# Kernel tuning notes

Measured on AMD Instinct MI355X. Metric: run time of the kernel, lower is better.

Reference implementation:

```python
import jax, jax.numpy as jnp
import numpy as np

E, L, R, H, V = 8, 8, 4, 4096, 32000
B, S = 2, 1024


def setup_inputs() -> dict:
    key = jax.random.key(0)
    ks = jax.random.split(key, 8)
    scale = 0.02
    return {
        "hidden_state": jax.random.normal(ks[0], (B, S, H), jnp.float32),
        "router_w": jax.random.normal(ks[1], (E, H), jnp.float32) * scale,
        "router_b": jnp.zeros((E,), jnp.float32),
        "expert_B": jax.random.normal(ks[2], (E, L, R, H), jnp.float32) * scale,
        "expert_A": jax.random.normal(ks[3], (E, L, H, R), jnp.float32) * scale,
        "deep_B": jax.random.normal(ks[4], (L, R, H), jnp.float32) * scale,
        "deep_A": jax.random.normal(ks[5], (L, H, R), jnp.float32) * scale,
        "lm_head_w": jax.random.normal(ks[6], (V, H), jnp.float32) * scale,
    }


def reference(hidden_state, router_w, router_b, expert_B, expert_A,
              deep_B, deep_A, lm_head_w):
    h = hidden_state  # [B,S,H]
    # Router applies softmax internally; forward softmaxes AGAIN (faithful to source).
    router_logits = jax.nn.softmax(
        jnp.einsum('bsh,eh->bse', h, router_w) + router_b, axis=-1)
    router_probs = jax.nn.softmax(router_logits, axis=-1)  # [B,S,E]
    psum = jnp.sum(router_probs, axis=-1, keepdims=True)   # [B,S,1] (== 1)

    n_layers = deep_B.shape[0]
    for i in range(n_layers):
        # All experts' LoRA low-rank projections in one batched contraction.
        z = jnp.einsum('bsh,erh->bser', h, expert_B[:, i])  # [B,S,E,r]
        # combined = sum_e p_e * (h + z_e @ A_e^T) = h * sum_e p_e + weighted delta
        zw = z * router_probs[..., None]                    # [B,S,E,r]
        delta = jnp.einsum('bser,ehr->bsh', zw, expert_A[:, i])
        combined = h * psum + delta                         # [B,S,H]
        # Residual deep LoRA merge: x + (x @ B^T) @ A^T
        low = jnp.einsum('bsh,rh->bsr', combined, deep_B[i])
        h = combined + jnp.einsum('bsr,hr->bsh', low, deep_A[i])

    lm_logits = jnp.einsum('bsh,vh->bsv', h, lm_head_w)  # [B,S,V]
    return (lm_logits, router_logits)
```

## Files before the change

kernel.cpp:

```cpp
#include <hip/hip_runtime.h>
#include <cstdint>
#include <cstddef>

#define HD 4096
#define EE 8
#define LL 8
#define RR 4
#define VV 32000
#define NTOK 2048
#define NKT (HD / 64)

typedef __attribute__((ext_vector_type(8))) short bf16x8;
typedef __attribute__((ext_vector_type(4))) float f32x4;

static __device__ __forceinline__ unsigned short f2bf(float f) {
    unsigned int u = __builtin_bit_cast(unsigned int, f);
    unsigned int r = (u + 0x7FFFu + ((u >> 16) & 1u)) >> 16;
    return (unsigned short)r;
}

__global__ __launch_bounds__(256) void fused_layers(
    const float* __restrict__ h_in,
    const float* __restrict__ router_w,
    const float* __restrict__ router_b,
    const float* __restrict__ expert_B,
    const float* __restrict__ expert_A,
    const float* __restrict__ deep_B,
    const float* __restrict__ deep_A,
    float* __restrict__ router_logits,
    unsigned short* __restrict__ h_out)
{
    __shared__ float h_lds[4][HD];
    __shared__ float zw_lds[4][32];
    __shared__ float probs_lds[4][EE];
    __shared__ float psum_lds[4];
    __shared__ float red[4][4][4];
    __shared__ float low_lds[4][4];

    const int tid  = threadIdx.x;
    const int lane = tid & 63;
    const int wv   = tid >> 6;
    const int t0   = blockIdx.x * 4;

    for (int t = 0; t < 4; ++t) {
        const float4* src = (const float4*)(h_in + (size_t)(t0 + t) * HD);
        float4* dst = (float4*)h_lds[t];
        #pragma unroll
        for (int q = 0; q < 4; ++q) dst[tid + q * 256] = src[tid + q * 256];
    }
    __syncthreads();

    {
        float racc[EE];
        #pragma unroll
        for (int e = 0; e < EE; ++e) racc[e] = 0.f;
        for (int k = 0; k < HD / 64; ++k) {
            int pos = lane + k * 64;
            float hv = h_lds[wv][pos];
            #pragma unroll
            for (int e = 0; e < EE; ++e) racc[e] += hv * router_w[e * HD + pos];
        }
        #pragma unroll
        for (int e = 0; e < EE; ++e)
            for (int m = 1; m < 64; m <<= 1) racc[e] += __shfl_xor(racc[e], m);
        if (lane == 0) {
            float lg[EE], mx = -1e30f;
            #pragma unroll
            for (int e = 0; e < EE; ++e) { lg[e] = racc[e] + router_b[e]; mx = fmaxf(mx, lg[e]); }
            float s = 0.f;
            #pragma unroll
            for (int e = 0; e < EE; ++e) { lg[e] = expf(lg[e] - mx); s += lg[e]; }
            float inv = 1.f / s;
            float p1[EE], mx2 = -1e30f;
            #pragma unroll
            for (int e = 0; e < EE; ++e) { p1[e] = lg[e] * inv; mx2 = fmaxf(mx2, p1[e]); }
            float s2 = 0.f, q2[EE];
            #pragma unroll
            for (int e = 0; e < EE; ++e) { q2[e] = expf(p1[e] - mx2); s2 += q2[e]; }
            float inv2 = 1.f / s2, ps = 0.f;
            #pragma unroll
            for (int e = 0; e < EE; ++e) {
                float p2 = q2[e] * inv2;
                probs_lds[wv][e] = p2;
                ps += p2;
                router_logits[(size_t)(t0 + wv) * EE + e] = p1[e];
            }
            psum_lds[wv] = ps;
        }
    }
    __syncthreads();

    for (int li = 0; li < LL; ++li) {
        {
            float zacc[8][4] = {};
            const float* bp[8];
            #pragma unroll
            for (int j = 0; j < 8; ++j) {
                int er = wv * 8 + j;
                int e = er >> 2, r = er & 3;
                bp[j] = expert_B + (size_t)(e * LL + li) * (RR * HD) + (size_t)r * HD;
            }
            for (int k = 0; k < 64; ++k) {
                int pos = lane + k * 64;
                float hv0 = h_lds[0][pos], hv1 = h_lds[1][pos];
                float hv2 = h_lds[2][pos], hv3 = h_lds[3][pos];
                #pragma unroll
                for (int j = 0; j < 8; ++j) {
                    float wt = bp[j][pos];
                    zacc[j][0] += wt * hv0; zacc[j][1] += wt * hv1;
                    zacc[j][2] += wt * hv2; zacc[j][3] += wt * hv3;
                }
            }
            #pragma unroll
            for (int j = 0; j < 8; ++j)
                #pragma unroll
                for (int t = 0; t < 4; ++t) {
                    float v = zacc[j][t];
                    for (int m = 1; m < 64; m <<= 1) v += __shfl_xor(v, m);
                    zacc[j][t] = v;
                }
            if (lane == 0) {
                #pragma unroll
                for (int j = 0; j < 8; ++j) {
                    int er = wv * 8 + j;
                    #pragma unroll
                    for (int t = 0; t < 4; ++t)
                        zw_lds[t][er] = zacc[j][t] * probs_lds[t][er >> 2];
                }
            }
        }
        __syncthreads();

        float dacc[4][16] = {};
        const int pbase = wv * 1024 + lane;
        for (int e = 0; e < EE; ++e) {
            float zwt[4][4];
            #pragma unroll
            for (int t = 0; t < 4; ++t)
                #pragma unroll
                for (int r = 0; r < RR; ++r) zwt[t][r] = zw_lds[t][e * 4 + r];
            const float4* ap = (const float4*)expert_A + (size_t)(e * LL + li) * HD;
            #pragma unroll
            for (int it = 0; it < 16; ++it) {
                float4 a4 = ap[pbase + it * 64];
                #pragma unroll
                for (int t = 0; t < 4; ++t)
                    dacc[t][it] += zwt[t][0] * a4.x + zwt[t][1] * a4.y +
                                   zwt[t][2] * a4.z + zwt[t][3] * a4.w;
            }
        }

        float lowacc[4][4] = {};
        float psv[4];
        #pragma unroll
        for (int t = 0; t < 4; ++t) psv[t] = psum_lds[t];
        const float* dbp = deep_B + (size_t)li * (RR * HD);
        #pragma unroll
        for (int it = 0; it < 16; ++it) {
            int pos = pbase + it * 64;
            float db0 = dbp[pos], db1 = dbp[HD + pos], db2 = dbp[2 * HD + pos], db3 = dbp[3 * HD + pos];
            #pragma unroll
            for (int t = 0; t < 4; ++t) {
                float c = h_lds[t][pos] * psv[t] + dacc[t][it];
                h_lds[t][pos] = c;
                lowacc[t][0] += c * db0; lowacc[t][1] += c * db1;
                lowacc[t][2] += c * db2; lowacc[t][3] += c * db3;
            }
        }
        #pragma unroll
        for (int t = 0; t < 4; ++t)
            #pragma unroll
            for (int r = 0; r < RR; ++r) {
                float v = lowacc[t][r];
                for (int m = 1; m < 64; m <<= 1) v += __shfl_xor(v, m);
                lowacc[t][r] = v;
            }
        if (lane == 0) {
            #pragma unroll
            for (int t = 0; t < 4; ++t)
                #pragma unroll
                for (int r = 0; r < RR; ++r) red[wv][t][r] = lowacc[t][r];
        }
        __syncthreads();
        if (tid < 16) {
            int t = tid >> 2, r = tid & 3;
            low_lds[t][r] = red[0][t][r] + red[1][t][r] + red[2][t][r] + red[3][t][r];
        }
        __syncthreads();

        {
            float lw[4][4];
            #pragma unroll
            for (int t = 0; t < 4; ++t)
                #pragma unroll
                for (int r = 0; r < RR; ++r) lw[t][r] = low_lds[t][r];
            const float4* dap = (const float4*)deep_A + (size_t)li * HD;
            #pragma unroll
            for (int it = 0; it < 16; ++it) {
                int pos = pbase + it * 64;
                float4 a4 = dap[pos];
                #pragma unroll
                for (int t = 0; t < 4; ++t)
                    h_lds[t][pos] += lw[t][0] * a4.x + lw[t][1] * a4.y +
                                     lw[t][2] * a4.z + lw[t][3] * a4.w;
            }
        }
        __syncthreads();
    }

    for (int t = 0; t < 4; ++t) {
        ushort4* dst = (ushort4*)(h_out + (size_t)(t0 + t) * HD);
        const float4* src = (const float4*)h_lds[t];
        #pragma unroll
        for (int q = 0; q < 4; ++q) {
            int c = tid + q * 256;
            float4 v = src[c];
            ushort4 o;
            o.x = f2bf(v.x); o.y = f2bf(v.y); o.z = f2bf(v.z); o.w = f2bf(v.w);
            dst[c] = o;
        }
    }
}

__global__ __launch_bounds__(256) void cvt_kernel(const float4* __restrict__ in,
                                                  ushort4* __restrict__ out, int n4)
{
    int i = blockIdx.x * 256 + threadIdx.x;
    int stride = gridDim.x * 256;
    for (; i < n4; i += stride) {
        float4 v = in[i];
        ushort4 o;
        o.x = f2bf(v.x); o.y = f2bf(v.y); o.z = f2bf(v.z); o.w = f2bf(v.w);
        out[i] = o;
    }
}

#define GLD(src, dst) __builtin_amdgcn_global_load_lds( \
    (const __attribute__((address_space(1))) unsigned int*)(src), \
    (__attribute__((address_space(3))) unsigned int*)(dst), 16, 0, 0)

#define STAGE(pp, matoff, bufv, hh, ktv) do { \
    char* db_ = smem + (bufv) * 65536 + (matoff) + (hh) * 16384 + wv * 1024; \
    GLD(pp[0] + (size_t)(hh) * (128ull * HD * 2) + (size_t)(ktv) * 128, db_); \
    GLD(pp[1] + (size_t)(hh) * (128ull * HD * 2) + (size_t)(ktv) * 128, db_ + 8192); \
} while (0)

#define LDSREAD(off) (*(const bf16x8*)(smem + (off)))

__global__ __launch_bounds__(512, 2) void lm_gemm256(
    const unsigned short* __restrict__ A,
    const unsigned short* __restrict__ Bw,
    float* __restrict__ C)
{
    __shared__ __attribute__((aligned(128))) char smem[131072];

    const int bid = blockIdx.x;
    const int swz = (bid & 7) * 125 + (bid >> 3);
    const int bm = swz & 7;
    const int bn = swz >> 3;

    const int tid  = threadIdx.x;
    const int lane = tid & 63;
    const int wv   = tid >> 6;
    const int wr   = wv >> 2;
    const int wc   = wv & 3;

    const char* pA[2];
    const char* pB[2];
    #pragma unroll
    for (int q = 0; q < 2; ++q) {
        int off = (q * 512 + tid) * 16;
        int p = off ^ (((off >> 9) & 1) << 5);
        int st = p >> 10;
        int r  = (st >> 1) * 16 + ((p >> 6) & 15);
        int cb = (st & 1) * 64 + (p & 63);
        pA[q] = (const char*)(A  + (size_t)(bm * 256 + r) * HD) + cb;
        pB[q] = (const char*)(Bw + (size_t)(bn * 256 + r) * HD) + cb;
    }

    const int xlane = ((lane >> 3) & 1) << 5;
    const int abase = ((wr * 8) << 11) + ((lane & 15) << 6) + ((lane >> 4) << 4);
    const int bbase = 32768 + ((wc * 4) << 11) + ((lane & 15) << 6) + ((lane >> 4) << 4);

    f32x4 acc[8][4] = {};
    bf16x8 aF[4][2], bF0[2][2], bF1[2][2];

    STAGE(pB, 32768, 0, 0, 0);
    STAGE(pB, 32768, 0, 1, 0);
    STAGE(pA, 0,     0, 0, 0);
    STAGE(pA, 0,     0, 1, 0);
    STAGE(pB, 32768, 1, 0, 1);
    STAGE(pB, 32768, 1, 1, 1);
    asm volatile("s_waitcnt vmcnt(4)" ::: "memory");
    __builtin_amdgcn_s_barrier();
    __builtin_amdgcn_sched_barrier(0);

    #pragma unroll 2
    for (int kt = 0; kt < NKT; ++kt) {
        const int cur = kt & 1;
        const int oth = cur ^ 1;
        const int cb0 = cur << 16;

        #pragma unroll
        for (int i = 0; i < 4; ++i)
            #pragma unroll
            for (int ks = 0; ks < 2; ++ks)
                aF[i][ks] = LDSREAD(cb0 + ((abase + (i << 11) + (ks << 10)) ^ xlane));
        #pragma unroll
        for (int n = 0; n < 2; ++n)
            #pragma unroll
            for (int ks = 0; ks < 2; ++ks)
                bF0[n][ks] = LDSREAD(cb0 + ((bbase + (n << 11) + (ks << 10)) ^ xlane));
        if (kt + 1 < NKT) STAGE(pA, 0, oth, 0, kt + 1);
        __builtin_amdgcn_s_barrier();
        __builtin_amdgcn_sched_barrier(0);
        __builtin_amdgcn_s_setprio(1);
        #pragma unroll
        for (int ks = 0; ks < 2; ++ks)
            #pragma unroll
            for (int i = 0; i < 4; ++i)
                #pragma unroll
                for (int n = 0; n < 2; ++n)
                    acc[i][n] = __builtin_amdgcn_mfma_f32_16x16x32_bf16(
                        aF[i][ks], bF0[n][ks], acc[i][n], 0, 0, 0);
        __builtin_amdgcn_s_setprio(0);
        __builtin_amdgcn_s_barrier();
        __builtin_amdgcn_sched_barrier(0);

        #pragma unroll
        for (int n = 0; n < 2; ++n)
            #pragma unroll
            for (int ks = 0; ks < 2; ++ks)
                bF1[n][ks] = LDSREAD(cb0 + ((bbase + ((n + 2) << 11) + (ks << 10)) ^ xlane));
        if (kt + 1 < NKT) STAGE(pA, 0, oth, 1, kt + 1);
        __builtin_amdgcn_s_barrier();
        __builtin_amdgcn_sched_barrier(0);
        __builtin_amdgcn_s_setprio(1);
        #pragma unroll
        for (int ks = 0; ks < 2; ++ks)
            #pragma unroll
            for (int i = 0; i < 4; ++i)
                #pragma unroll
                for (int n = 0; n < 2; ++n)
                    acc[i][n + 2] = __builtin_amdgcn_mfma_f32_16x16x32_bf16(
                        aF[i][ks], bF1[n][ks], acc[i][n + 2], 0, 0, 0);
        __builtin_amdgcn_s_setprio(0);
        __builtin_amdgcn_s_barrier();
        __builtin_amdgcn_sched_barrier(0);

        #pragma unroll
        for (int i = 0; i < 4; ++i)
            #pragma unroll
            for (int ks = 0; ks < 2; ++ks)
                aF[i][ks] = LDSREAD(cb0 + ((abase + ((i + 4) << 11) + (ks << 10)) ^ xlane));
        if (kt + 2 < NKT) STAGE(pB, 32768, cur, 0, kt + 2);
        __builtin_amdgcn_s_barrier();
        __builtin_amdgcn_sched_barrier(0);
        __builtin_amdgcn_s_setprio(1);
        #pragma unroll
        for (int ks = 0; ks < 2; ++ks)
            #pragma unroll
            for (int i = 0; i < 4; ++i)
                #pragma unroll
                for (int n = 0; n < 2; ++n)
                    acc[i + 4][n + 2] = __builtin_amdgcn_mfma_f32_16x16x32_bf16(
                        aF[i][ks], bF1[n][ks], acc[i + 4][n + 2], 0, 0, 0);
        __builtin_amdgcn_s_setprio(0);
        __builtin_amdgcn_s_barrier();
        __builtin_amdgcn_sched_barrier(0);

        if (kt + 2 < NKT) {
            STAGE(pB, 32768, cur, 1, kt + 2);
            asm volatile("s_waitcnt vmcnt(4)" ::: "memory");
        } else {
            asm volatile("s_waitcnt vmcnt(0)" ::: "memory");
        }
        __builtin_amdgcn_s_barrier();
        __builtin_amdgcn_sched_barrier(0);
        __builtin_amdgcn_s_setprio(1);
        #pragma unroll
        for (int ks = 0; ks < 2; ++ks)
            #pragma unroll
            for (int i = 0; i < 4; ++i)
                #pragma unroll
                for (int n = 0; n < 2; ++n)
                    acc[i + 4][n] = __builtin_amdgcn_mfma_f32_16x16x32_bf16(
                        aF[i][ks], bF0[n][ks], acc[i + 4][n], 0, 0, 0);
        __builtin_amdgcn_s_setprio(0);
        __builtin_amdgcn_s_barrier();
        __builtin_amdgcn_sched_barrier(0);
    }

    const int crow0 = bm * 256 + wr * 128 + ((lane >> 4) << 2);
    const int ccol0 = bn * 256 + wc * 64 + (lane & 15);
    #pragma unroll
    for (int fm = 0; fm < 8; ++fm)
        #pragma unroll
        for (int fn = 0; fn < 4; ++fn) {
            int row = crow0 + fm * 16;
            int col = ccol0 + fn * 16;
            #pragma unroll
            for (int j = 0; j < 4; ++j)
                C[(size_t)(row + j) * VV + col] = acc[fm][fn][j];
        }
}

extern "C" void kernel_launch(void* const* d_in, const int* in_sizes, int n_in,
                              void* d_out, int out_size, void* d_ws, size_t ws_size,
                              hipStream_t stream) {
    const float* h_in      = (const float*)d_in[0];
    const float* router_w  = (const float*)d_in[1];
    const float* router_b  = (const float*)d_in[2];
    const float* expert_B  = (const float*)d_in[3];
    const float* expert_A  = (const float*)d_in[4];
    const float* deep_B    = (const float*)d_in[5];
    const float* deep_A    = (const float*)d_in[6];
    const float* lm_head_w = (const float*)d_in[7];

    float* out = (float*)d_out;
    float* router_logits_out = out + (size_t)NTOK * VV;

    unsigned short* h_bf = (unsigned short*)d_ws;
    unsigned short* w_bf = (unsigned short*)((char*)d_ws + (size_t)NTOK * HD * 2);

    fused_layers<<<dim3(NTOK / 4), dim3(256), 0, stream>>>(
        h_in, router_w, router_b, expert_B, expert_A, deep_B, deep_A,
        router_logits_out, h_bf);

    cvt_kernel<<<dim3(4096), dim3(256), 0, stream>>>(
        (const float4*)lm_head_w, (ushort4*)w_bf, VV * HD / 4);

    lm_gemm256<<<dim3((NTOK / 256) * (VV / 256)), dim3(512), 0, stream>>>(
        h_bf, w_bf, out);
}
```

Before: 1.068 ms.

## Fuse weight conversion into layer kernel and prefetch B fragments in GEMM

Merges the lm_head fp32-to-bf16 conversion kernel into the per-token layer kernel, with blocks split by index between conversion and layer work, so both run concurrently and one launch is dropped. The layer kernel moves to 512 threads with float4 vectorised loads for the router and expert_B projections, halving per-wave work. Separately, the GEMM double-buffers the bF0 fragments and loads the next tile's B fragments early to hide LDS latency. The risks are higher register pressure in the GEMM and load imbalance between conversion and layer blocks.

```diff
diff --git a/kernel.cpp b/kernel.cpp
--- a/kernel.cpp
+++ b/kernel.cpp
@@ -9,6 +9,7 @@
 #define VV 32000
 #define NTOK 2048
 #define NKT (HD / 64)
+#define CVTB 2048
 
 typedef __attribute__((ext_vector_type(8))) short bf16x8;
 typedef __attribute__((ext_vector_type(4))) float f32x4;
@@ -19,7 +20,7 @@
     return (unsigned short)r;
 }
 
-__global__ __launch_bounds__(256) void fused_layers(
+__global__ __launch_bounds__(512, 4) void fused_all(
     const float* __restrict__ h_in,
     const float* __restrict__ router_w,
     const float* __restrict__ router_b,
@@ -28,37 +29,58 @@
     const float* __restrict__ deep_B,
     const float* __restrict__ deep_A,
     float* __restrict__ router_logits,
-    unsigned short* __restrict__ h_out)
+    unsigned short* __restrict__ h_out,
+    const float4* __restrict__ lm_w,
+    ushort4* __restrict__ w_bf)
 {
     __shared__ float h_lds[4][HD];
     __shared__ float zw_lds[4][32];
     __shared__ float probs_lds[4][EE];
     __shared__ float psum_lds[4];
-    __shared__ float red[4][4][4];
+    __shared__ float red[8][4][4];
     __shared__ float low_lds[4][4];
 
-    const int tid  = threadIdx.x;
+    const int bid = blockIdx.x;
+    const int tid = threadIdx.x;
+
+    if (!((bid < 1024) && ((bid & 1) == 0))) {
+        const int ci = (bid < 1024) ? (bid >> 1) : (512 + (bid - 1024));
+        const int n4 = VV * HD / 4;
+        const int stride = CVTB * 512;
+        for (int i = ci * 512 + tid; i < n4; i += stride) {
+            float4 v = lm_w[i];
+            ushort4 o;
+            o.x = f2bf(v.x); o.y = f2bf(v.y); o.z = f2bf(v.z); o.w = f2bf(v.w);
+            w_bf[i] = o;
+        }
+        return;
+    }
+
     const int lane = tid & 63;
     const int wv   = tid >> 6;
-    const int t0   = blockIdx.x * 4;
+    const int t0   = (bid >> 1) * 4;
 
     for (int t = 0; t < 4; ++t) {
         const float4* src = (const float4*)(h_in + (size_t)(t0 + t) * HD);
         float4* dst = (float4*)h_lds[t];
         #pragma unroll
-        for (int q = 0; q < 4; ++q) dst[tid + q * 256] = src[tid + q * 256];
+        for (int q = 0; q < 2; ++q) dst[tid + q * 512] = src[tid + q * 512];
     }
     __syncthreads();
 
-    {
+    if (wv < 4) {
         float racc[EE];
         #pragma unroll
         for (int e = 0; e < EE; ++e) racc[e] = 0.f;
-        for (int k = 0; k < HD / 64; ++k) {
-            int pos = lane + k * 64;
-            float hv = h_lds[wv][pos];
-            #pragma unroll
-            for (int e = 0; e < EE; ++e) racc[e] += hv * router_w[e * HD + pos];
+        const float4* h4 = (const float4*)h_lds[wv];
+        for (int k4 = 0; k4 < HD / 256; ++k4) {
+            int idx = lane + k4 * 64;
+            float4 hv = h4[idx];
+            #pragma unroll
+            for (int e = 0; e < EE; ++e) {
+                float4 w4 = ((const float4*)(router_w + e * HD))[idx];
+                racc[e] += w4.x * hv.x + w4.y * hv.y + w4.z * hv.z + w4.w * hv.w;
+            }
         }
         #pragma unroll
         for (int e = 0; e < EE; ++e)
@@ -92,27 +114,32 @@
 
     for (int li = 0; li < LL; ++li) {
         {
-            float zacc[8][4] = {};
-            const float* bp[8];
-            #pragma unroll
-            for (int j = 0; j < 8; ++j) {
-                int er = wv * 8 + j;
+            float zacc[4][4] = {};
+            const float4* bp4[4];
+            #pragma unroll
+            for (int j = 0; j < 4; ++j) {
+                int er = wv * 4 + j;
                 int e = er >> 2, r = er & 3;
-                bp[j] = expert_B + (size_t)(e * LL + li) * (RR * HD) + (size_t)r * HD;
-            }
-            for (int k = 0; k < 64; ++k) {
-                int pos = lane + k * 64;
-                float hv0 = h_lds[0][pos], hv1 = h_lds[1][pos];
-                float hv2 = h_lds[2][pos], hv3 = h_lds[3][pos];
-                #pragma unroll
-                for (int j = 0; j < 8; ++j) {
-                    float wt = bp[j][pos];
-                    zacc[j][0] += wt * hv0; zacc[j][1] += wt * hv1;
-                    zacc[j][2] += wt * hv2; zacc[j][3] += wt * hv3;
+                bp4[j] = (const float4*)(expert_B + (size_t)((e * LL + li) * RR + r) * HD);
+            }
+            const float4* h40 = (const float4*)h_lds[0];
+            const float4* h41 = (const float4*)h_lds[1];
+            const float4* h42 = (const float4*)h_lds[2];
+            const float4* h43 = (const float4*)h_lds[3];
+            for (int k4 = 0; k4 < HD / 256; ++k4) {
+                int idx = lane + k4 * 64;
+                float4 hv0 = h40[idx], hv1 = h41[idx], hv2 = h42[idx], hv3 = h43[idx];
+                #pragma unroll
+                for (int j = 0; j < 4; ++j) {
+                    float4 w4 = bp4[j][idx];
+                    zacc[j][0] += w4.x * hv0.x + w4.y * hv0.y + w4.z * hv0.z + w4.w * hv0.w;
+                    zacc[j][1] += w4.x * hv1.x + w4.y * hv1.y + w4.z * hv1.z + w4.w * hv1.w;
+                    zacc[j][2] += w4.x * hv2.x + w4.y * hv2.y + w4.z * hv2.z + w4.w * hv2.w;
+                    zacc[j][3] += w4.x * hv3.x + w4.y * hv3.y + w4.z * hv3.z + w4.w * hv3.w;
                 }
             }
             #pragma unroll
-            for (int j = 0; j < 8; ++j)
+            for (int j = 0; j < 4; ++j)
                 #pragma unroll
                 for (int t = 0; t < 4; ++t) {
                     float v = zacc[j][t];
@@ -121,8 +148,8 @@
                 }
             if (lane == 0) {
                 #pragma unroll
-                for (int j = 0; j < 8; ++j) {
-                    int er = wv * 8 + j;
+                for (int j = 0; j < 4; ++j) {
+                    int er = wv * 4 + j;
                     #pragma unroll
                     for (int t = 0; t < 4; ++t)
                         zw_lds[t][er] = zacc[j][t] * probs_lds[t][er >> 2];
@@ -131,8 +158,8 @@
         }
         __syncthreads();
 
-        float dacc[4][16] = {};
-        const int pbase = wv * 1024 + lane;
+        float dacc[4][8] = {};
+        const int pbase = wv * 512 + lane;
         for (int e = 0; e < EE; ++e) {
             float zwt[4][4];
             #pragma unroll
@@ -141,7 +168,7 @@
                 for (int r = 0; r < RR; ++r) zwt[t][r] = zw_lds[t][e * 4 + r];
             const float4* ap = (const float4*)expert_A + (size_t)(e * LL + li) * HD;
             #pragma unroll
-            for (int it = 0; it < 16; ++it) {
+            for (int it = 0; it < 8; ++it) {
                 float4 a4 = ap[pbase + it * 64];
                 #pragma unroll
                 for (int t = 0; t < 4; ++t)
@@ -156,7 +183,7 @@
         for (int t = 0; t < 4; ++t) psv[t] = psum_lds[t];
         const float* dbp = deep_B + (size_t)li * (RR * HD);
         #pragma unroll
-        for (int it = 0; it < 16; ++it) {
+        for (int it = 0; it < 8; ++it) {
             int pos = pbase + it * 64;
             float db0 = dbp[pos], db1 = dbp[HD + pos], db2 = dbp[2 * HD + pos], db3 = dbp[3 * HD + pos];
             #pragma unroll
@@ -184,7 +211,10 @@
         __syncthreads();
         if (tid < 16) {
             int t = tid >> 2, r = tid & 3;
-            low_lds[t][r] = red[0][t][r] + red[1][t][r] + red[2][t][r] + red[3][t][r];
+            float s = 0.f;
+            #pragma unroll
+            for (int w = 0; w < 8; ++w) s += red[w][t][r];
+            low_lds[t][r] = s;
         }
         __syncthreads();
 
@@ -196,7 +226,7 @@
                 for (int r = 0; r < RR; ++r) lw[t][r] = low_lds[t][r];
             const float4* dap = (const float4*)deep_A + (size_t)li * HD;
             #pragma unroll
-            for (int it = 0; it < 16; ++it) {
+            for (int it = 0; it < 8; ++it) {
                 int pos = pbase + it * 64;
                 float4 a4 = dap[pos];
                 #pragma unroll
@@ -212,26 +242,13 @@
         ushort4* dst = (ushort4*)(h_out + (size_t)(t0 + t) * HD);
         const float4* src = (const float4*)h_lds[t];
         #pragma unroll
-        for (int q = 0; q < 4; ++q) {
-            int c = tid + q * 256;
+        for (int q = 0; q < 2; ++q) {
+            int c = tid + q * 512;
             float4 v = src[c];
             ushort4 o;
             o.x = f2bf(v.x); o.y = f2bf(v.y); o.z = f2bf(v.z); o.w = f2bf(v.w);
             dst[c] = o;
         }
-    }
-}
-
-__global__ __launch_bounds__(256) void cvt_kernel(const float4* __restrict__ in,
-                                                  ushort4* __restrict__ out, int n4)
-{
-    int i = blockIdx.x * 256 + threadIdx.x;
-    int stride = gridDim.x * 256;
-    for (; i < n4; i += stride) {
-        float4 v = in[i];
-        ushort4 o;
-        o.x = f2bf(v.x); o.y = f2bf(v.y); o.z = f2bf(v.z); o.w = f2bf(v.w);
-        out[i] = o;
     }
 }
 
@@ -283,7 +300,7 @@
     const int bbase = 32768 + ((wc * 4) << 11) + ((lane & 15) << 6) + ((lane >> 4) << 4);
 
     f32x4 acc[8][4] = {};
-    bf16x8 aF[4][2], bF0[2][2], bF1[2][2];
+    bf16x8 aF[4][2], bF0[2][2][2], bF1[2][2];
 
     STAGE(pB, 32768, 0, 0, 0);
     STAGE(pB, 32768, 0, 1, 0);
@@ -294,6 +311,11 @@
     asm volatile("s_waitcnt vmcnt(4)" ::: "memory");
     __builtin_amdgcn_s_barrier();
     __builtin_amdgcn_sched_barrier(0);
+    #pragma unroll
+    for (int n = 0; n < 2; ++n)
+        #pragma unroll
+        for (int ks = 0; ks < 2; ++ks)
+            bF0[0][n][ks] = LDSREAD(((bbase + (n << 11) + (ks << 10)) ^ xlane));
 
     #pragma unroll 2
     for (int kt = 0; kt < NKT; ++kt) {
@@ -306,11 +328,6 @@
             #pragma unroll
             for (int ks = 0; ks < 2; ++ks)
                 aF[i][ks] = LDSREAD(cb0 + ((abase + (i << 11) + (ks << 10)) ^ xlane));
-        #pragma unroll
-        for (int n = 0; n < 2; ++n)
-            #pragma unroll
-            for (int ks = 0; ks < 2; ++ks)
-                bF0[n][ks] = LDSREAD(cb0 + ((bbase + (n << 11) + (ks << 10)) ^ xlane));
         if (kt + 1 < NKT) STAGE(pA, 0, oth, 0, kt + 1);
         __builtin_amdgcn_s_barrier();
         __builtin_amdgcn_sched_barrier(0);
@@ -322,7 +339,7 @@
                 #pragma unroll
                 for (int n = 0; n < 2; ++n)
                     acc[i][n] = __builtin_amdgcn_mfma_f32_16x16x32_bf16(
-                        aF[i][ks], bF0[n][ks], acc[i][n], 0, 0, 0);
+                        aF[i][ks], bF0[cur][n][ks], acc[i][n], 0, 0, 0);
         __builtin_amdgcn_s_setprio(0);
         __builtin_amdgcn_s_barrier();
         __builtin_amdgcn_sched_barrier(0);
@@ -377,6 +394,14 @@
         }
         __builtin_amdgcn_s_barrier();
         __builtin_amdgcn_sched_barrier(0);
+        if (kt + 1 < NKT) {
+            const int nb0 = oth << 16;
+            #pragma unroll
+            for (int n = 0; n < 2; ++n)
+                #pragma unroll
+                for (int ks = 0; ks < 2; ++ks)
+                    bF0[oth][n][ks] = LDSREAD(nb0 + ((bbase + (n << 11) + (ks << 10)) ^ xlane));
+        }
         __builtin_amdgcn_s_setprio(1);
         #pragma unroll
         for (int ks = 0; ks < 2; ++ks)
@@ -385,7 +410,7 @@
                 #pragma unroll
                 for (int n = 0; n < 2; ++n)
                     acc[i + 4][n] = __builtin_amdgcn_mfma_f32_16x16x32_bf16(
-                        aF[i][ks], bF0[n][ks], acc[i + 4][n], 0, 0, 0);
+                        aF[i][ks], bF0[cur][n][ks], acc[i + 4][n], 0, 0, 0);
         __builtin_amdgcn_s_setprio(0);
         __builtin_amdgcn_s_barrier();
         __builtin_amdgcn_sched_barrier(0);
@@ -423,12 +448,9 @@
     unsigned short* h_bf = (unsigned short*)d_ws;
     unsigned short* w_bf = (unsigned short*)((char*)d_ws + (size_t)NTOK * HD * 2);
 
-    fused_layers<<<dim3(NTOK / 4), dim3(256), 0, stream>>>(
+    fused_all<<<dim3(1024 + CVTB), dim3(512), 0, stream>>>(
         h_in, router_w, router_b, expert_B, expert_A, deep_B, deep_A,
-        router_logits_out, h_bf);
-
-    cvt_kernel<<<dim3(4096), dim3(256), 0, stream>>>(
-        (const float4*)lm_head_w, (ushort4*)w_bf, VV * HD / 4);
+        router_logits_out, h_bf, (const float4*)lm_head_w, (ushort4*)w_bf);
 
     lm_gemm256<<<dim3((NTOK / 256) * (VV / 256)), dim3(512), 0, stream>>>(
         h_bf, w_bf, out);
```

After: 2.129 ms. 99.3% more time.
